# Kernel optimization log

Measured on AMD Instinct MI355X. Metric: run time of the kernel, lower is better.

## Reference

```python
import jax, jax.numpy as jnp
import numpy as np

N_NODES = 50000
N_EDGES = 800000
IN_C = 128
OUT_C = 128
BN_EPS = 1e-5


def setup_inputs() -> dict:
    key = jax.random.key(0)
    ks = jax.random.split(key, 4)
    x = jax.random.normal(ks[0], (N_NODES, IN_C), dtype=jnp.float32)
    edge_index = jax.random.randint(ks[1], (2, N_EDGES), 0, N_NODES, dtype=jnp.int64)
    W1 = jax.random.normal(ks[2], (2 * IN_C, OUT_C), dtype=jnp.float32) * (1.0 / np.sqrt(2 * IN_C))
    b1 = jnp.zeros((OUT_C,), dtype=jnp.float32)
    W2 = jax.random.normal(ks[3], (OUT_C, OUT_C), dtype=jnp.float32) * (1.0 / np.sqrt(OUT_C))
    b2 = jnp.zeros((OUT_C,), dtype=jnp.float32)
    gamma = jnp.ones((OUT_C,), dtype=jnp.float32)
    beta = jnp.zeros((OUT_C,), dtype=jnp.float32)
    return {"x": x, "edge_index": edge_index, "W1": W1, "b1": b1,
            "W2": W2, "b2": b2, "gamma": gamma, "beta": beta}


def reference(x, edge_index, W1, b1, W2, b2, gamma, beta):
    # EdgeConv (PyG): message = mlp(cat([x_i, x_j - x_i])), max-aggregated onto target i.
    # edge_index[0] = source j, edge_index[1] = target i (source_to_target flow).
    src, dst = edge_index[0], edge_index[1]
    x_i = x[dst]                      # [E, C] gather (target)
    x_j = x[src]                      # [E, C] gather (source)
    m = jnp.concatenate([x_i, x_j - x_i], axis=-1)  # [E, 2C]
    h = jax.nn.relu(m @ W1 + b1) @ W2 + b2          # [E, out]
    agg = jax.ops.segment_max(h, dst, num_segments=x.shape[0])  # scatter-max
    # nodes with no incoming edges -> fill 0 (matches scatter_max default fill)
    agg = jnp.where(jnp.isfinite(agg), agg, jnp.zeros_like(agg))
    # BatchNorm1d, training mode: batch stats over nodes, biased variance, eps=1e-5
    mean = jnp.mean(agg, axis=0)
    var = jnp.mean(jnp.square(agg - mean), axis=0)
    out = (agg - mean) * jax.lax.rsqrt(var + BN_EPS) * gamma + beta
    return out
```

## Files before the change

### kernel.cpp

```cpp
#include <hip/hip_runtime.h>
#include <hip/hip_fp16.h>
#include <math.h>

#define IN_C 128
#define OUT_C 128
#define BN_EPS 1e-5f
#define NODES2 64

typedef __fp16 f16x8 __attribute__((ext_vector_type(8)));
typedef __fp16 f16x2 __attribute__((ext_vector_type(2)));
typedef float f32x4 __attribute__((ext_vector_type(4)));

__global__ __launch_bounds__(256) void k_zero(int* __restrict__ deg, int n,
                                              float* __restrict__ stats) {
    int idx = blockIdx.x * blockDim.x + threadIdx.x;
    int stride = gridDim.x * blockDim.x;
    for (int i = idx; i < n; i += stride) deg[i] = 0;
    if (blockIdx.x == 0 && threadIdx.x < 256) stats[threadIdx.x] = 0.0f;
}

__global__ __launch_bounds__(256) void k_hist(const int* __restrict__ edst,
                                              int* __restrict__ deg, int E) {
    int idx = blockIdx.x * blockDim.x + threadIdx.x;
    int stride = gridDim.x * blockDim.x;
    for (int e = idx; e < E; e += stride) atomicAdd(&deg[edst[e]], 1);
}

__global__ __launch_bounds__(1024) void k_scan(const int* __restrict__ deg,
                                               int* __restrict__ rowptr,
                                               int* __restrict__ cursor, int n) {
    __shared__ int wsum[16], woff[16], ctot;
    int t = threadIdx.x, lane = t & 63, wv = t >> 6;
    int carry = 0;
    for (int base = 0; base < n; base += 1024) {
        int i = base + t;
        int v = (i < n) ? deg[i] : 0;
        int x = v;
#pragma unroll
        for (int off = 1; off < 64; off <<= 1) {
            int u = __shfl_up(x, off, 64);
            if (lane >= off) x += u;
        }
        if (lane == 63) wsum[wv] = x;
        __syncthreads();
        if (wv == 0 && lane < 16) {
            int y = wsum[lane];
#pragma unroll
            for (int off = 1; off < 16; off <<= 1) {
                int u = __shfl_up(y, off, 16);
                if ((lane & 15) >= off) y += u;
            }
            woff[lane] = y - wsum[lane];
            if (lane == 15) ctot = y;
        }
        __syncthreads();
        int excl = carry + x + woff[wv] - v;
        if (i < n) { rowptr[i] = excl; cursor[i] = excl; }
        carry += ctot;
        __syncthreads();
    }
    if (t == 0) rowptr[n] = carry;
}

__global__ __launch_bounds__(256) void k_scatter(const int* __restrict__ esrc,
                                                 const int* __restrict__ edst,
                                                 int* __restrict__ cursor,
                                                 int* __restrict__ ssrc, int E) {
    int idx = blockIdx.x * blockDim.x + threadIdx.x;
    int stride = gridDim.x * blockDim.x;
    for (int e = idx; e < E; e += stride) {
        int pos = atomicAdd(&cursor[edst[e]], 1);
        ssrc[pos] = esrc[e];
    }
}

__global__ __launch_bounds__(256) void k_node(const float* __restrict__ x,
                                              const float* __restrict__ W1,
                                              const float* __restrict__ b1,
                                              float* __restrict__ A,
                                              float* __restrict__ Bm,
                                              int n_nodes) {
    __shared__ float xs[NODES2][IN_C];
    int t = threadIdx.x;
    int c = t & 127;
    bool isA = (t < 128);
    float bias = b1[c];
    for (int base = blockIdx.x * NODES2; base < n_nodes;
         base += gridDim.x * NODES2) {
        int nn = min(NODES2, n_nodes - base);
        __syncthreads();
        for (int i = t; i < nn * IN_C; i += 256) {
            int n = i >> 7, k = i & 127;
            xs[n][k] = x[(size_t)(base + n) * IN_C + k];
        }
        __syncthreads();
        float acc[NODES2];
#pragma unroll
        for (int n = 0; n < NODES2; n++) acc[n] = 0.0f;
        for (int kh = 0; kh < IN_C; kh += 4) {
            float w[4];
#pragma unroll
            for (int j = 0; j < 4; j++) {
                float wbot = W1[(size_t)(kh + j + 128) * OUT_C + c];
                w[j] = isA ? (W1[(size_t)(kh + j) * OUT_C + c] - wbot) : wbot;
            }
#pragma unroll
            for (int n = 0; n < NODES2; n++) {
                float4 xv = *(const float4*)&xs[n][kh];
                acc[n] = fmaf(xv.x, w[0], acc[n]);
                acc[n] = fmaf(xv.y, w[1], acc[n]);
                acc[n] = fmaf(xv.z, w[2], acc[n]);
                acc[n] = fmaf(xv.w, w[3], acc[n]);
            }
        }
        float* dst = isA ? A : Bm;
        float add = isA ? bias : 0.0f;
        for (int n = 0; n < nn; n++)
            dst[(size_t)(base + n) * OUT_C + c] = acc[n] + add;
    }
}

__global__ __launch_bounds__(256) void k_edge(const float* __restrict__ A,
                                              const float* __restrict__ Bm,
                                              const int* __restrict__ rowptr,
                                              const int* __restrict__ ssrc,
                                              const float* __restrict__ W2,
                                              const float* __restrict__ b2,
                                              float* __restrict__ out,
                                              float* __restrict__ gsum,
                                              float* __restrict__ gsumsq,
                                              int n_nodes) {
    __shared__ __fp16 w2t[128 * 128];
    __shared__ __fp16 rt[4 * 16 * 128];
    __shared__ float ssum[128], ssq[128];

    int t = threadIdx.x, lane = t & 63;
    int wv = t >> 6;
    int mrow = lane & 15, kgrp = lane >> 4;

    for (int idx = t; idx < 64 * 128; idx += 256) {
        int kp = idx >> 7, n = idx & 127;
        float w0 = W2[(size_t)(2 * kp) * OUT_C + n];
        float w1 = W2[(size_t)(2 * kp + 1) * OUT_C + n];
        f16x2 p = __builtin_amdgcn_cvt_pkrtz(w0, w1);
        *(f16x2*)&w2t[n * 128 + ((2 * kp + 8 * n) & 127)] = p;
    }
    if (t < 128) { ssum[t] = 0.0f; ssq[t] = 0.0f; }
    float b2r[8];
#pragma unroll
    for (int nt = 0; nt < 8; nt++) b2r[nt] = b2[nt * 16 + mrow];
    __syncthreads();

    __fp16* rtw = &rt[wv * 16 * 128];
    int gwave = blockIdx.x * 4 + wv;
    int nw = gridDim.x * 4;

    for (int i = gwave; i < n_nodes; i += nw) {
        int rbase = rowptr[i], rend = rowptr[i + 1];
        int d = rend - rbase;
        if (d == 0) {
            if (kgrp == 0) {
#pragma unroll
                for (int nt = 0; nt < 8; nt++)
                    out[(size_t)i * OUT_C + nt * 16 + mrow] = 0.0f;
            }
            continue;
        }
        float2 av = *(const float2*)&A[(size_t)i * OUT_C + 2 * lane];
        float vmax[8];
#pragma unroll
        for (int nt = 0; nt < 8; nt++) vmax[nt] = -INFINITY;

        for (int c0 = 0; c0 < d; c0 += 16) {
            int idxs = rbase + c0 + (lane & 15);
            if (idxs >= rend) idxs = rend - 1;
            int sid = ssrc[idxs];
            int nrows = min(16, d - c0);
            float2 bvs[16];
#pragma unroll
            for (int e = 0; e < 16; e++) {
                int jj = __builtin_amdgcn_readlane(sid, e);
                bvs[e] = *(const float2*)&Bm[(size_t)jj * OUT_C + 2 * lane];
            }
#pragma unroll
            for (int e = 0; e < 16; e++) {
                float r0 = fmaxf(av.x + bvs[e].x, 0.0f);
                float r1 = fmaxf(av.y + bvs[e].y, 0.0f);
                f16x2 p = __builtin_amdgcn_cvt_pkrtz(r0, r1);
                *(f16x2*)&rtw[e * 128 + ((2 * lane + 8 * e) & 127)] = p;
            }
            f32x4 acc[8];
#pragma unroll
            for (int nt = 0; nt < 8; nt++) acc[nt] = (f32x4){0.f, 0.f, 0.f, 0.f};
#pragma unroll
            for (int kk = 0; kk < 4; kk++) {
                int k0 = kk * 32 + kgrp * 8;
                f16x8 a0 = *(f16x8*)&rtw[mrow * 128 + ((k0 + 8 * mrow) & 127)];
#pragma unroll
                for (int nt = 0; nt < 8; nt++) {
                    int rr = nt * 16 + mrow;
                    f16x8 bf = *(f16x8*)&w2t[rr * 128 + ((k0 + 8 * rr) & 127)];
                    acc[nt] = __builtin_amdgcn_mfma_f32_16x16x32_f16(a0, bf, acc[nt], 0, 0, 0);
                }
            }
#pragma unroll
            for (int nt = 0; nt < 8; nt++) {
#pragma unroll
                for (int reg = 0; reg < 4; reg++) {
                    int rl = kgrp * 4 + reg;
                    if (rl < nrows) vmax[nt] = fmaxf(vmax[nt], acc[nt][reg]);
                }
            }
        }
#pragma unroll
        for (int nt = 0; nt < 8; nt++) {
            float v = vmax[nt];
            v = fmaxf(v, __shfl_xor(v, 16, 64));
            v = fmaxf(v, __shfl_xor(v, 32, 64));
            vmax[nt] = v;
        }
        if (kgrp == 0) {
#pragma unroll
            for (int nt = 0; nt < 8; nt++) {
                float v = vmax[nt] + b2r[nt];
                out[(size_t)i * OUT_C + nt * 16 + mrow] = v;
                atomicAdd(&ssum[nt * 16 + mrow], v);
                atomicAdd(&ssq[nt * 16 + mrow], v * v);
            }
        }
    }
    __syncthreads();
    if (t < 128) {
        atomicAdd(&gsum[t], ssum[t]);
        atomicAdd(&gsumsq[t], ssq[t]);
    }
}

__global__ __launch_bounds__(128) void k_finalize(const float* __restrict__ gsum,
                                                  const float* __restrict__ gsumsq,
                                                  const float* __restrict__ gamma,
                                                  const float* __restrict__ beta,
                                                  float* __restrict__ scale,
                                                  float* __restrict__ shift,
                                                  int n_nodes) {
    int c = threadIdx.x;
    if (c < OUT_C) {
        float inv_n = 1.0f / (float)n_nodes;
        float mean = gsum[c] * inv_n;
        float var = fmaxf(gsumsq[c] * inv_n - mean * mean, 0.0f);
        float sc = gamma[c] * rsqrtf(var + BN_EPS);
        scale[c] = sc;
        shift[c] = beta[c] - mean * sc;
    }
}

__global__ __launch_bounds__(256) void k_norm(float* __restrict__ out,
                                              const float* __restrict__ scale,
                                              const float* __restrict__ shift,
                                              int n_vec) {
    int idx = blockIdx.x * blockDim.x + threadIdx.x;
    int stride = gridDim.x * blockDim.x;
    for (int i = idx; i < n_vec; i += stride) {
        float4 v = ((const float4*)out)[i];
        int c = (i * 4) & 127;
        float4 sc = *(const float4*)&scale[c];
        float4 sh = *(const float4*)&shift[c];
        v.x = fmaf(v.x, sc.x, sh.x);
        v.y = fmaf(v.y, sc.y, sh.y);
        v.z = fmaf(v.z, sc.z, sh.z);
        v.w = fmaf(v.w, sc.w, sh.w);
        ((float4*)out)[i] = v;
    }
}

extern "C" void kernel_launch(void* const* d_in, const int* in_sizes, int n_in,
                              void* d_out, int out_size, void* d_ws, size_t ws_size,
                              hipStream_t stream) {
    const float* x     = (const float*)d_in[0];
    const int*   ei    = (const int*)d_in[1];
    const float* W1    = (const float*)d_in[2];
    const float* b1    = (const float*)d_in[3];
    const float* W2    = (const float*)d_in[4];
    const float* b2    = (const float*)d_in[5];
    const float* gamma = (const float*)d_in[6];
    const float* beta  = (const float*)d_in[7];

    int n_nodes = in_sizes[0] / IN_C;
    int n_edges = in_sizes[1] / 2;
    const int* esrc = ei;
    const int* edst = ei + n_edges;

    float* out = (float*)d_out;
    float* A   = (float*)d_ws;
    float* Bm  = A + (size_t)n_nodes * OUT_C;
    float* stats = Bm + (size_t)n_nodes * OUT_C;
    float* gsum   = stats;
    float* gsumsq = stats + 128;
    float* scale  = stats + 256;
    float* shift  = stats + 384;
    int* deg    = (int*)(stats + 512);
    int* rowptr = deg + n_nodes;
    int* cursor = rowptr + n_nodes + 1;
    int* ssrc   = cursor + n_nodes;

    k_zero<<<256, 256, 0, stream>>>(deg, n_nodes, stats);
    k_hist<<<1024, 256, 0, stream>>>(edst, deg, n_edges);
    k_scan<<<1, 1024, 0, stream>>>(deg, rowptr, cursor, n_nodes);
    k_scatter<<<1024, 256, 0, stream>>>(esrc, edst, cursor, ssrc, n_edges);
    k_node<<<(n_nodes + NODES2 - 1) / NODES2, 256, 0, stream>>>(x, W1, b1, A, Bm, n_nodes);
    k_edge<<<768, 256, 0, stream>>>(A, Bm, rowptr, ssrc, W2, b2,
                                    out, gsum, gsumsq, n_nodes);
    k_finalize<<<1, 128, 0, stream>>>(gsum, gsumsq, gamma, beta, scale, shift, n_nodes);
    k_norm<<<2048, 256, 0, stream>>>(out, scale, shift, n_nodes * OUT_C / 4);
}
```

Measured before the change: 558.9 us.

## Parallelize CSR scan into three kernels and store gathered node term in fp16

Replaces the single-block serial prefix scan over node degrees with a three-pass multi-block scan (per-block scan, block-sum scan, offset add). Separately, the per-source node projection Bm is now stored in fp16 instead of fp32, which halves the bytes gathered per edge in the edge kernel. The fp16 storage lowers the precision of the first-layer term before ReLU, and the block-sum scan assumes there are at most 256 blocks.

```diff
diff --git a/kernel.cpp b/kernel.cpp
--- a/kernel.cpp
+++ b/kernel.cpp
@@ -6,6 +6,7 @@
 #define OUT_C 128
 #define BN_EPS 1e-5f
 #define NODES2 64
+#define SCAN_CHUNK 256
 
 typedef __fp16 f16x8 __attribute__((ext_vector_type(8)));
 typedef __fp16 f16x2 __attribute__((ext_vector_type(2)));
@@ -26,40 +27,61 @@
     for (int e = idx; e < E; e += stride) atomicAdd(&deg[edst[e]], 1);
 }
 
-__global__ __launch_bounds__(1024) void k_scan(const int* __restrict__ deg,
+__global__ __launch_bounds__(256) void k_scan1(const int* __restrict__ deg,
                                                int* __restrict__ rowptr,
+                                               int* __restrict__ bsum, int n) {
+    __shared__ int ws4[4];
+    int t = threadIdx.x, lane = t & 63, wv = t >> 6;
+    int i = blockIdx.x * SCAN_CHUNK + t;
+    int v = (i < n) ? deg[i] : 0;
+    int x = v;
+#pragma unroll
+    for (int off = 1; off < 64; off <<= 1) {
+        int u = __shfl_up(x, off, 64);
+        if (lane >= off) x += u;
+    }
+    if (lane == 63) ws4[wv] = x;
+    __syncthreads();
+    int woff = 0;
+#pragma unroll
+    for (int k = 0; k < 3; k++) if (k < wv) woff += ws4[k];
+    int excl = woff + x - v;
+    if (i < n) rowptr[i] = excl;
+    if (t == 255) bsum[blockIdx.x] = woff + x;
+}
+
+__global__ __launch_bounds__(256) void k_scan2(const int* __restrict__ bsum,
+                                               int* __restrict__ boff,
+                                               int* __restrict__ rowptr,
+                                               int NB, int n) {
+    __shared__ int ws4[4];
+    int t = threadIdx.x, lane = t & 63, wv = t >> 6;
+    int v = (t < NB) ? bsum[t] : 0;
+    int x = v;
+#pragma unroll
+    for (int off = 1; off < 64; off <<= 1) {
+        int u = __shfl_up(x, off, 64);
+        if (lane >= off) x += u;
+    }
+    if (lane == 63) ws4[wv] = x;
+    __syncthreads();
+    int woff = 0;
+#pragma unroll
+    for (int k = 0; k < 3; k++) if (k < wv) woff += ws4[k];
+    int excl = woff + x - v;
+    if (t < NB) boff[t] = excl;
+    if (t == NB - 1) rowptr[n] = excl + v;
+}
+
+__global__ __launch_bounds__(256) void k_scan3(int* __restrict__ rowptr,
+                                               const int* __restrict__ boff,
                                                int* __restrict__ cursor, int n) {
-    __shared__ int wsum[16], woff[16], ctot;
-    int t = threadIdx.x, lane = t & 63, wv = t >> 6;
-    int carry = 0;
-    for (int base = 0; base < n; base += 1024) {
-        int i = base + t;
-        int v = (i < n) ? deg[i] : 0;
-        int x = v;
-#pragma unroll
-        for (int off = 1; off < 64; off <<= 1) {
-            int u = __shfl_up(x, off, 64);
-            if (lane >= off) x += u;
-        }
-        if (lane == 63) wsum[wv] = x;
-        __syncthreads();
-        if (wv == 0 && lane < 16) {
-            int y = wsum[lane];
-#pragma unroll
-            for (int off = 1; off < 16; off <<= 1) {
-                int u = __shfl_up(y, off, 16);
-                if ((lane & 15) >= off) y += u;
-            }
-            woff[lane] = y - wsum[lane];
-            if (lane == 15) ctot = y;
-        }
-        __syncthreads();
-        int excl = carry + x + woff[wv] - v;
-        if (i < n) { rowptr[i] = excl; cursor[i] = excl; }
-        carry += ctot;
-        __syncthreads();
-    }
-    if (t == 0) rowptr[n] = carry;
+    int i = blockIdx.x * SCAN_CHUNK + threadIdx.x;
+    if (i < n) {
+        int r = rowptr[i] + boff[blockIdx.x];
+        rowptr[i] = r;
+        cursor[i] = r;
+    }
 }
 
 __global__ __launch_bounds__(256) void k_scatter(const int* __restrict__ esrc,
@@ -78,7 +100,7 @@
                                               const float* __restrict__ W1,
                                               const float* __restrict__ b1,
                                               float* __restrict__ A,
-                                              float* __restrict__ Bm,
+                                              __fp16* __restrict__ Bm,
                                               int n_nodes) {
     __shared__ float xs[NODES2][IN_C];
     int t = threadIdx.x;
@@ -113,15 +135,18 @@
                 acc[n] = fmaf(xv.w, w[3], acc[n]);
             }
         }
-        float* dst = isA ? A : Bm;
-        float add = isA ? bias : 0.0f;
-        for (int n = 0; n < nn; n++)
-            dst[(size_t)(base + n) * OUT_C + c] = acc[n] + add;
+        if (isA) {
+            for (int n = 0; n < nn; n++)
+                A[(size_t)(base + n) * OUT_C + c] = acc[n] + bias;
+        } else {
+            for (int n = 0; n < nn; n++)
+                Bm[(size_t)(base + n) * OUT_C + c] = (__fp16)acc[n];
+        }
     }
 }
 
 __global__ __launch_bounds__(256) void k_edge(const float* __restrict__ A,
-                                              const float* __restrict__ Bm,
+                                              const __fp16* __restrict__ Bm,
                                               const int* __restrict__ rowptr,
                                               const int* __restrict__ ssrc,
                                               const float* __restrict__ W2,
@@ -176,16 +201,16 @@
             if (idxs >= rend) idxs = rend - 1;
             int sid = ssrc[idxs];
             int nrows = min(16, d - c0);
-            float2 bvs[16];
+            f16x2 bvs[16];
 #pragma unroll
             for (int e = 0; e < 16; e++) {
                 int jj = __builtin_amdgcn_readlane(sid, e);
-                bvs[e] = *(const float2*)&Bm[(size_t)jj * OUT_C + 2 * lane];
+                bvs[e] = *(const f16x2*)&Bm[(size_t)jj * OUT_C + 2 * lane];
             }
 #pragma unroll
             for (int e = 0; e < 16; e++) {
-                float r0 = fmaxf(av.x + bvs[e].x, 0.0f);
-                float r1 = fmaxf(av.y + bvs[e].y, 0.0f);
+                float r0 = fmaxf(av.x + (float)bvs[e].x, 0.0f);
+                float r1 = fmaxf(av.y + (float)bvs[e].y, 0.0f);
                 f16x2 p = __builtin_amdgcn_cvt_pkrtz(r0, r1);
                 *(f16x2*)&rtw[e * 128 + ((2 * lane + 8 * e) & 127)] = p;
             }
@@ -292,8 +317,8 @@
 
     float* out = (float*)d_out;
     float* A   = (float*)d_ws;
-    float* Bm  = A + (size_t)n_nodes * OUT_C;
-    float* stats = Bm + (size_t)n_nodes * OUT_C;
+    __fp16* Bm = (__fp16*)(A + (size_t)n_nodes * OUT_C);
+    float* stats = (float*)(Bm + (size_t)n_nodes * OUT_C);
     float* gsum   = stats;
     float* gsumsq = stats + 128;
     float* scale  = stats + 256;
@@ -302,10 +327,15 @@
     int* rowptr = deg + n_nodes;
     int* cursor = rowptr + n_nodes + 1;
     int* ssrc   = cursor + n_nodes;
+    int* bsum   = ssrc + n_edges;
+    int NB = (n_nodes + SCAN_CHUNK - 1) / SCAN_CHUNK;
+    int* boff   = bsum + NB;
 
     k_zero<<<256, 256, 0, stream>>>(deg, n_nodes, stats);
     k_hist<<<1024, 256, 0, stream>>>(edst, deg, n_edges);
-    k_scan<<<1, 1024, 0, stream>>>(deg, rowptr, cursor, n_nodes);
+    k_scan1<<<NB, 256, 0, stream>>>(deg, rowptr, bsum, n_nodes);
+    k_scan2<<<1, 256, 0, stream>>>(bsum, boff, rowptr, NB, n_nodes);
+    k_scan3<<<NB, 256, 0, stream>>>(rowptr, boff, cursor, n_nodes);
     k_scatter<<<1024, 256, 0, stream>>>(esrc, edst, cursor, ssrc, n_edges);
     k_node<<<(n_nodes + NODES2 - 1) / NODES2, 256, 0, stream>>>(x, W1, b1, A, Bm, n_nodes);
     k_edge<<<768, 256, 0, stream>>>(A, Bm, rowptr, ssrc, W2, b2,
```

Result: faster. 517.9 us (-7.3%).
